# Performance work log

Hardware: AMD Instinct MI355X
Metric: run time of the kernel (lower is better)

Reference implementation:

```python
import jax, jax.numpy as jnp
import numpy as np

# attn_reps = "8x0n+30x1n": per head channel C = 8 scalars + 30 Lorentz four-vectors (4 each) = 128
N_SCALARS, N_VECTORS = 8, 30
ETA = jnp.diag(jnp.array([1.0, -1.0, -1.0, -1.0], dtype=jnp.float32))  # Minkowski metric


def _quat_to_rot(q):
    # q: (M,4) unit quaternions -> (M,3,3) rotation matrices
    w, x, y, z = q[:, 0], q[:, 1], q[:, 2], q[:, 3]
    r0 = jnp.stack([1 - 2 * (y * y + z * z), 2 * (x * y - w * z), 2 * (x * z + w * y)], axis=-1)
    r1 = jnp.stack([2 * (x * y + w * z), 1 - 2 * (x * x + z * z), 2 * (y * z - w * x)], axis=-1)
    r2 = jnp.stack([2 * (x * z - w * y), 2 * (y * z + w * x), 1 - 2 * (x * x + y * y)], axis=-1)
    return jnp.stack([r0, r1, r2], axis=-2)


def _random_lorentz(key, M):
    # random proper Lorentz transforms: boost(beta) @ blockdiag(1, R)
    k1, k2 = jax.random.split(key)
    quat = jax.random.normal(k1, (M, 4), dtype=jnp.float32)
    quat = quat / jnp.linalg.norm(quat, axis=-1, keepdims=True)
    R = _quat_to_rot(quat)  # (M,3,3)
    beta = jax.random.uniform(k2, (M, 3), minval=-1.0, maxval=1.0, dtype=jnp.float32) * (0.6 / np.sqrt(3.0))
    b2 = jnp.sum(beta * beta, axis=-1)  # (M,), < 0.36
    gamma = 1.0 / jnp.sqrt(1.0 - b2)
    n = beta / jnp.sqrt(jnp.maximum(b2, 1e-12))[:, None]
    gb = gamma[:, None] * beta  # (M,3)
    top = jnp.concatenate([gamma[:, None], gb], axis=-1)[:, None, :]  # (M,1,4)
    spatial = jnp.eye(3, dtype=jnp.float32) + (gamma - 1.0)[:, None, None] * n[:, :, None] * n[:, None, :]
    bottom = jnp.concatenate([gb[:, :, None], spatial], axis=-1)  # (M,3,4)
    B = jnp.concatenate([top, bottom], axis=-2)  # (M,4,4) boost
    rot4 = jnp.zeros((M, 4, 4), dtype=jnp.float32).at[:, 0, 0].set(1.0).at[:, 1:, 1:].set(R)
    return jnp.einsum('mij,mjk->mik', B, rot4)


def setup_inputs() -> dict:
    key = jax.random.key(0)
    kq, kk, kv, kl = jax.random.split(key, 4)
    B, H, N, C = 8, 8, 1024, 128
    q = jax.random.normal(kq, (B, H, N, C), dtype=jnp.float32)
    k = jax.random.normal(kk, (B, H, N, C), dtype=jnp.float32)
    v = jax.random.normal(kv, (B, H, N, C), dtype=jnp.float32)
    L = _random_lorentz(kl, B * N).reshape(B, N, 4, 4)
    return {"q_local": q, "k_local": k, "v_local": v, "lframes_matrices": L}


def _transform(x, M):
    # TensorRepsTransform: scalars pass through, four-vectors get v' = M v (per particle)
    # x: (B,H,N,C), M: (B,N,4,4)
    s = x[..., :N_SCALARS]
    vec = x[..., N_SCALARS:].reshape(x.shape[:-1] + (N_VECTORS, 4))
    vec = jnp.einsum('bnij,bhnvj->bhnvi', M, vec)
    return jnp.concatenate([s, vec.reshape(x.shape[:-1] + (N_VECTORS * 4,))], axis=-1)


def reference(q_local, k_local, v_local, lframes_matrices):
    C = q_local.shape[-1]
    # InverseLFrames: Lorentz inverse  Lambda^{-1} = eta Lambda^T eta
    inv = jnp.einsum('ij,bnkj,kl->bnil', ETA, lframes_matrices, ETA)
    # LowerIndices: lower the output index -> eta @ Lambda^{-1}
    lower_inv = jnp.einsum('ij,bnjk->bnik', ETA, inv)
    q_g = _transform(q_local, inv)
    k_g = _transform(k_local, lower_inv)
    v_g = _transform(v_local, inv)
    # standard SDPA (scale 1/sqrt(C))
    scores = jnp.einsum('bhqc,bhkc->bhqk', q_g, k_g) * (1.0 / np.sqrt(C))
    attn = jax.nn.softmax(scores, axis=-1)
    out_g = jnp.einsum('bhqk,bhkc->bhqc', attn, v_g)
    # back to local frame with Lambda itself
    return _transform(out_g, lframes_matrices)
```

## Files before the change

kernel.cpp:

```cpp
#include <hip/hip_runtime.h>
#include <math.h>

typedef _Float16 f16;
typedef _Float16 f16x4 __attribute__((ext_vector_type(4)));
typedef _Float16 f16x8 __attribute__((ext_vector_type(8)));
typedef float    f32x4 __attribute__((ext_vector_type(4)));

typedef const __attribute__((address_space(1))) void gv_t;
typedef __attribute__((address_space(3))) void lv_t;

#define NSEQ 1024
#define CD   128
#define LT   136


__global__ __launch_bounds__(256)
void ipa_pre(const float* __restrict__ kg, const float* __restrict__ vg,
             const float* __restrict__ Lm, f16* __restrict__ khs, f16* __restrict__ vhs)
{
    __shared__ float LL[64 * 16];
    __shared__ __align__(16) f16 Kt[64 * LT];
    __shared__ __align__(16) f16 Vt[64 * LT];
    const int bx = blockIdx.x, nt = blockIdx.y, tid = threadIdx.x;
    const int bh = ((bx & 7) << 3) | (bx >> 3);
    const int b  = bh >> 3;
    const float* Lb = Lm + ((size_t)b * NSEQ + nt * 64) * 16;
    for (int t = tid; t < 64 * 16; t += 256) LL[t] = Lb[t];
    __syncthreads();

    const size_t base = ((size_t)bh * NSEQ + nt * 64) * CD;
    #pragma unroll
    for (int it = 0; it < 8; ++it) {
        int g = it * 256 + tid;
        int row = g >> 5, cg = g & 31;
        size_t idx = base + row * CD + cg * 4;
        const float* Lr = &LL[row * 16];
        float4 xk = *(const float4*)(kg + idx);
        float4 xv = *(const float4*)(vg + idx);
        float4 yk = xk, yv = xv;
        if (cg >= 2) {
            float t0 = xk.x, t1 = -xk.y, t2 = -xk.z, t3 = -xk.w;
            yk.x = Lr[0]*t0 + Lr[4]*t1 + Lr[8] *t2 + Lr[12]*t3;
            yk.y = Lr[1]*t0 + Lr[5]*t1 + Lr[9] *t2 + Lr[13]*t3;
            yk.z = Lr[2]*t0 + Lr[6]*t1 + Lr[10]*t2 + Lr[14]*t3;
            yk.w = Lr[3]*t0 + Lr[7]*t1 + Lr[11]*t2 + Lr[15]*t3;
            t0 = xv.x; t1 = -xv.y; t2 = -xv.z; t3 = -xv.w;
            yv.x =  (Lr[0]*t0 + Lr[4]*t1 + Lr[8] *t2 + Lr[12]*t3);
            yv.y = -(Lr[1]*t0 + Lr[5]*t1 + Lr[9] *t2 + Lr[13]*t3);
            yv.z = -(Lr[2]*t0 + Lr[6]*t1 + Lr[10]*t2 + Lr[14]*t3);
            yv.w = -(Lr[3]*t0 + Lr[7]*t1 + Lr[11]*t2 + Lr[15]*t3);
        }
        f16x4 hk = {(f16)yk.x, (f16)yk.y, (f16)yk.z, (f16)yk.w};
        f16x4 hv = {(f16)yv.x, (f16)yv.y, (f16)yv.z, (f16)yv.w};
        *(f16x4*)&Kt[row * LT + cg * 4] = hk;
        *(f16x4*)&Vt[row * LT + cg * 4] = hv;
    }
    __syncthreads();

    f16* kout = khs + (size_t)bh * 131072 + (size_t)nt * 4 * 4 * 512;
    #pragma unroll
    for (int it = 0; it < 4; ++it) {
        int slot = it * 256 + tid;
        int g16l = slot >> 8, cs = (slot >> 6) & 3, L = slot & 63;
        int lq = L & 15, quad = L >> 4;
        int keyl = ((g16l >> 1) << 5) + ((lq >> 2) << 3) + ((g16l & 1) << 2) + (lq & 3);
        f16x8 kv = *(const f16x8*)&Kt[keyl * LT + cs * 32 + quad * 8];
        *(f16x8*)(kout + (g16l * 4 + cs) * 512 + L * 8) = kv;
    }
    f16* vout = vhs + (size_t)bh * 131072 + (size_t)nt * 2 * 8 * 512;
    #pragma unroll
    for (int it = 0; it < 4; ++it) {
        int slot = it * 256 + tid;
        int k32l = slot >> 9, cb = (slot >> 6) & 7, L = slot & 63;
        int lq = L & 15, quad = L >> 4;
        int c = cb * 16 + lq;
        f16x8 o;
        #pragma unroll
        for (int j = 0; j < 8; ++j)
            o[j] = Vt[(k32l * 32 + quad * 8 + j) * LT + c];
        *(f16x8*)(vout + (k32l * 8 + cb) * 512 + L * 8) = o;
    }
}

__global__ __launch_bounds__(256, 2)
void ipa_attn(const float* __restrict__ qg, const f16* __restrict__ khs,
              const f16* __restrict__ vhs, const float* __restrict__ Lm,
              float* __restrict__ out)
{
    __shared__ __align__(16) f16 sK[2][8192];
    __shared__ __align__(16) f16 sV[2][8192];
    const int n = blockIdx.x;
    const int bh = ((n & 7) << 3) | ((n >> 3) & 7);
    const int b  = bh >> 3;
    const int tid = threadIdx.x;
    const int w = tid >> 6, lane = tid & 63, lq = lane & 15, quad = lane >> 4;
    const int qblk = n >> 6;
    const int q0 = qblk * 128 + w * 32;
    const f16* kbh = khs + (size_t)bh * 131072;
    const f16* vbh = vhs + (size_t)bh * 131072;
    const float sc2 = 0.12751744154226873f;

    auto stage = [&](int nb, int it) {
        const char* kp = (const char*)(kbh + (size_t)it * 8192);
        const char* vp = (const char*)(vbh + (size_t)it * 8192);
        char* kd = (char*)&sK[nb][0];
        char* vd = (char*)&sV[nb][0];
        #pragma unroll
        for (int j = 0; j < 4; ++j) {
            int off = (w * 4 + j) * 1024;
            __builtin_amdgcn_global_load_lds((gv_t*)(kp + off + lane * 16),
                                             (lv_t*)(kd + off), 16, 0, 0);
            __builtin_amdgcn_global_load_lds((gv_t*)(vp + off + lane * 16),
                                             (lv_t*)(vd + off), 16, 0, 0);
        }
    };

    f16x8 qf[2][4];
    #pragma unroll
    for (int u = 0; u < 2; ++u) {
        int qrow = q0 + u * 16 + lq;
        const float* Lr = Lm + ((size_t)b * NSEQ + qrow) * 16;
        const float* qp = qg + ((size_t)bh * NSEQ + qrow) * CD;
        float Lv[16];
        #pragma unroll
        for (int i = 0; i < 4; ++i) *(float4*)&Lv[i*4] = *(const float4*)(Lr + i*4);
        #pragma unroll
        for (int cs = 0; cs < 4; ++cs) {
            int c0 = cs * 32 + quad * 8;
            float4 x0 = *(const float4*)(qp + c0);
            float4 x1 = *(const float4*)(qp + c0 + 4);
            if (c0 >= 8) {
                float t0 = x0.x, t1 = -x0.y, t2 = -x0.z, t3 = -x0.w;
                float4 y;
                y.x =  (Lv[0]*t0 + Lv[4]*t1 + Lv[8] *t2 + Lv[12]*t3);
                y.y = -(Lv[1]*t0 + Lv[5]*t1 + Lv[9] *t2 + Lv[13]*t3);
                y.z = -(Lv[2]*t0 + Lv[6]*t1 + Lv[10]*t2 + Lv[14]*t3);
                y.w = -(Lv[3]*t0 + Lv[7]*t1 + Lv[11]*t2 + Lv[15]*t3);
                x0 = y;
                t0 = x1.x; t1 = -x1.y; t2 = -x1.z; t3 = -x1.w;
                y.x =  (Lv[0]*t0 + Lv[4]*t1 + Lv[8] *t2 + Lv[12]*t3);
                y.y = -(Lv[1]*t0 + Lv[5]*t1 + Lv[9] *t2 + Lv[13]*t3);
                y.z = -(Lv[2]*t0 + Lv[6]*t1 + Lv[10]*t2 + Lv[14]*t3);
                y.w = -(Lv[3]*t0 + Lv[7]*t1 + Lv[11]*t2 + Lv[15]*t3);
                x1 = y;
            }
            qf[u][cs] = (f16x8){(f16)(x0.x*sc2), (f16)(x0.y*sc2), (f16)(x0.z*sc2), (f16)(x0.w*sc2),
                                (f16)(x1.x*sc2), (f16)(x1.y*sc2), (f16)(x1.z*sc2), (f16)(x1.w*sc2)};
        }
    }

    f32x4 oacc[2][8];
    #pragma unroll
    for (int u = 0; u < 2; ++u)
        #pragma unroll
        for (int cb = 0; cb < 8; ++cb) oacc[u][cb] = (f32x4){0.f, 0.f, 0.f, 0.f};
    float mrun[2] = {-1e30f, -1e30f}, lrun[2] = {0.f, 0.f};

    stage(0, 0);

    for (int it = 0; it < 16; ++it) {
        const int cur = it & 1;
        __syncthreads();
        if (it < 15) stage(cur ^ 1, it + 1);

        const f16* kb = &sK[cur][0];
        const f16* vb = &sV[cur][0];
        f16x8 kf[4][4];
        #pragma unroll
        for (int g = 0; g < 4; ++g)
            #pragma unroll
            for (int cs = 0; cs < 4; ++cs)
                kf[g][cs] = *(const f16x8*)&kb[(g * 4 + cs) * 512 + lane * 8];

        f32x4 s[2][4];
        #pragma unroll
        for (int u = 0; u < 2; ++u)
            #pragma unroll
            for (int g = 0; g < 4; ++g) s[u][g] = (f32x4){0.f, 0.f, 0.f, 0.f};
        #pragma unroll
        for (int g = 0; g < 4; ++g)
            #pragma unroll
            for (int cs = 0; cs < 4; ++cs) {
                s[0][g] = __builtin_amdgcn_mfma_f32_16x16x32_f16(kf[g][cs], qf[0][cs], s[0][g], 0, 0, 0);
                s[1][g] = __builtin_amdgcn_mfma_f32_16x16x32_f16(kf[g][cs], qf[1][cs], s[1][g], 0, 0, 0);
            }

        f16x8 vf[2][8];
        #pragma unroll
        for (int k2 = 0; k2 < 2; ++k2)
            #pragma unroll
            for (int cb = 0; cb < 8; ++cb)
                vf[k2][cb] = *(const f16x8*)&vb[(k2 * 8 + cb) * 512 + lane * 8];

        f16x8 pf[2][2];
        #pragma unroll
        for (int u = 0; u < 2; ++u) {
            float mx = -1e30f;
            #pragma unroll
            for (int g = 0; g < 4; ++g)
                mx = fmaxf(mx, fmaxf(fmaxf(s[u][g].x, s[u][g].y), fmaxf(s[u][g].z, s[u][g].w)));
            mx = fmaxf(mx, __shfl_xor(mx, 16, 64));
            mx = fmaxf(mx, __shfl_xor(mx, 32, 64));
            float mnew = fmaxf(mrun[u], mx);
            if (!__all(mx <= mrun[u])) {
                float alpha = exp2f(mrun[u] - mnew);
                lrun[u] *= alpha;
                #pragma unroll
                for (int cb = 0; cb < 8; ++cb) oacc[u][cb] *= alpha;
                mrun[u] = mnew;
            }
            float p[16], rs = 0.f;
            #pragma unroll
            for (int g = 0; g < 4; ++g) {
                p[g*4+0] = exp2f(s[u][g].x - mnew);
                p[g*4+1] = exp2f(s[u][g].y - mnew);
                p[g*4+2] = exp2f(s[u][g].z - mnew);
                p[g*4+3] = exp2f(s[u][g].w - mnew);
                rs += (p[g*4+0] + p[g*4+1]) + (p[g*4+2] + p[g*4+3]);
            }
            rs += __shfl_xor(rs, 16, 64);
            rs += __shfl_xor(rs, 32, 64);
            lrun[u] += rs;
            pf[u][0] = (f16x8){(f16)p[0],(f16)p[1],(f16)p[2],(f16)p[3],(f16)p[4],(f16)p[5],(f16)p[6],(f16)p[7]};
            pf[u][1] = (f16x8){(f16)p[8],(f16)p[9],(f16)p[10],(f16)p[11],(f16)p[12],(f16)p[13],(f16)p[14],(f16)p[15]};
        }
        #pragma unroll
        for (int k2 = 0; k2 < 2; ++k2)
            #pragma unroll
            for (int cb = 0; cb < 8; ++cb) {
                oacc[0][cb] = __builtin_amdgcn_mfma_f32_16x16x32_f16(vf[k2][cb], pf[0][k2], oacc[0][cb], 0, 0, 0);
                oacc[1][cb] = __builtin_amdgcn_mfma_f32_16x16x32_f16(vf[k2][cb], pf[1][k2], oacc[1][cb], 0, 0, 0);
            }
    }

    #pragma unroll
    for (int u = 0; u < 2; ++u) {
        int qrow = q0 + u * 16 + lq;
        float invl = 1.0f / lrun[u];
        const float* Lr = Lm + ((size_t)b * NSEQ + qrow) * 16;
        float* ob = out + ((size_t)bh * NSEQ + qrow) * CD;
        #pragma unroll
        for (int cb = 0; cb < 8; ++cb) {
            int c0 = cb * 16 + quad * 4;
            float o0 = oacc[u][cb].x*invl, o1 = oacc[u][cb].y*invl;
            float o2 = oacc[u][cb].z*invl, o3 = oacc[u][cb].w*invl;
            float4 r;
            if (c0 >= 8) {
                r.x = Lr[0] *o0 + Lr[1] *o1 + Lr[2] *o2 + Lr[3] *o3;
                r.y = Lr[4] *o0 + Lr[5] *o1 + Lr[6] *o2 + Lr[7] *o3;
                r.z = Lr[8] *o0 + Lr[9] *o1 + Lr[10]*o2 + Lr[11]*o3;
                r.w = Lr[12]*o0 + Lr[13]*o1 + Lr[14]*o2 + Lr[15]*o3;
            } else {
                r.x = o0; r.y = o1; r.z = o2; r.w = o3;
            }
            *(float4*)(ob + c0) = r;
        }
    }
}

extern "C" void kernel_launch(void* const* d_in, const int* in_sizes, int n_in,
                              void* d_out, int out_size, void* d_ws, size_t ws_size,
                              hipStream_t stream) {
    const float* q = (const float*)d_in[0];
    const float* k = (const float*)d_in[1];
    const float* v = (const float*)d_in[2];
    const float* L = (const float*)d_in[3];
    float* o = (float*)d_out;
    f16* khs = (f16*)d_ws;
    f16* vhs = khs + (size_t)64 * 131072;
    dim3 grid1(64, 16);
    ipa_pre<<<grid1, 256, 0, stream>>>(k, v, L, khs, vhs);
    ipa_attn<<<512, 256, 0, stream>>>(q, khs, vhs, L, o);
}
```

Baseline: 190.3 us.

## Halve attention query and KV tile sizes and double the grid

```diff
diff --git a/kernel.cpp b/kernel.cpp
--- a/kernel.cpp
+++ b/kernel.cpp
@@ -87,27 +87,27 @@
               const f16* __restrict__ vhs, const float* __restrict__ Lm,
               float* __restrict__ out)
 {
-    __shared__ __align__(16) f16 sK[2][8192];
-    __shared__ __align__(16) f16 sV[2][8192];
+    __shared__ __align__(16) f16 sK[2][4096];
+    __shared__ __align__(16) f16 sV[2][4096];
     const int n = blockIdx.x;
     const int bh = ((n & 7) << 3) | ((n >> 3) & 7);
     const int b  = bh >> 3;
     const int tid = threadIdx.x;
     const int w = tid >> 6, lane = tid & 63, lq = lane & 15, quad = lane >> 4;
     const int qblk = n >> 6;
-    const int q0 = qblk * 128 + w * 32;
+    const int q0 = qblk * 64 + w * 16;
     const f16* kbh = khs + (size_t)bh * 131072;
     const f16* vbh = vhs + (size_t)bh * 131072;
     const float sc2 = 0.12751744154226873f;
 
     auto stage = [&](int nb, int it) {
-        const char* kp = (const char*)(kbh + (size_t)it * 8192);
-        const char* vp = (const char*)(vbh + (size_t)it * 8192);
+        const char* kp = (const char*)(kbh + (size_t)it * 4096);
+        const char* vp = (const char*)(vbh + (size_t)it * 4096);
         char* kd = (char*)&sK[nb][0];
         char* vd = (char*)&sV[nb][0];
         #pragma unroll
-        for (int j = 0; j < 4; ++j) {
-            int off = (w * 4 + j) * 1024;
+        for (int j = 0; j < 2; ++j) {
+            int off = (w * 2 + j) * 1024;
             __builtin_amdgcn_global_load_lds((gv_t*)(kp + off + lane * 16),
                                              (lv_t*)(kd + off), 16, 0, 0);
             __builtin_amdgcn_global_load_lds((gv_t*)(vp + off + lane * 16),
@@ -115,10 +115,9 @@
         }
     };
 
-    f16x8 qf[2][4];
-    #pragma unroll
-    for (int u = 0; u < 2; ++u) {
-        int qrow = q0 + u * 16 + lq;
+    f16x8 qf[4];
+    {
+        int qrow = q0 + lq;
         const float* Lr = Lm + ((size_t)b * NSEQ + qrow) * 16;
         const float* qp = qg + ((size_t)bh * NSEQ + qrow) * CD;
         float Lv[16];
@@ -144,106 +143,78 @@
                 y.w = -(Lv[3]*t0 + Lv[7]*t1 + Lv[11]*t2 + Lv[15]*t3);
                 x1 = y;
             }
-            qf[u][cs] = (f16x8){(f16)(x0.x*sc2), (f16)(x0.y*sc2), (f16)(x0.z*sc2), (f16)(x0.w*sc2),
-                                (f16)(x1.x*sc2), (f16)(x1.y*sc2), (f16)(x1.z*sc2), (f16)(x1.w*sc2)};
-        }
-    }
-
-    f32x4 oacc[2][8];
-    #pragma unroll
-    for (int u = 0; u < 2; ++u)
-        #pragma unroll
-        for (int cb = 0; cb < 8; ++cb) oacc[u][cb] = (f32x4){0.f, 0.f, 0.f, 0.f};
-    float mrun[2] = {-1e30f, -1e30f}, lrun[2] = {0.f, 0.f};
+            qf[cs] = (f16x8){(f16)(x0.x*sc2), (f16)(x0.y*sc2), (f16)(x0.z*sc2), (f16)(x0.w*sc2),
+                             (f16)(x1.x*sc2), (f16)(x1.y*sc2), (f16)(x1.z*sc2), (f16)(x1.w*sc2)};
+        }
+    }
+
+    f32x4 oacc[8];
+    #pragma unroll
+    for (int cb = 0; cb < 8; ++cb) oacc[cb] = (f32x4){0.f, 0.f, 0.f, 0.f};
+    float mrun = -1e30f, lrun = 0.f;
 
     stage(0, 0);
 
-    for (int it = 0; it < 16; ++it) {
+    for (int it = 0; it < 32; ++it) {
         const int cur = it & 1;
         __syncthreads();
-        if (it < 15) stage(cur ^ 1, it + 1);
+        if (it < 31) stage(cur ^ 1, it + 1);
 
         const f16* kb = &sK[cur][0];
         const f16* vb = &sV[cur][0];
-        f16x8 kf[4][4];
-        #pragma unroll
-        for (int g = 0; g < 4; ++g)
+
+        f32x4 s[2];
+        s[0] = (f32x4){0.f, 0.f, 0.f, 0.f};
+        s[1] = (f32x4){0.f, 0.f, 0.f, 0.f};
+        #pragma unroll
+        for (int cs = 0; cs < 4; ++cs) {
+            f16x8 kf0 = *(const f16x8*)&kb[(cs    ) * 512 + lane * 8];
+            f16x8 kf1 = *(const f16x8*)&kb[(cs + 4) * 512 + lane * 8];
+            s[0] = __builtin_amdgcn_mfma_f32_16x16x32_f16(kf0, qf[cs], s[0], 0, 0, 0);
+            s[1] = __builtin_amdgcn_mfma_f32_16x16x32_f16(kf1, qf[cs], s[1], 0, 0, 0);
+        }
+
+        float mx = fmaxf(fmaxf(fmaxf(s[0].x, s[0].y), fmaxf(s[0].z, s[0].w)),
+                         fmaxf(fmaxf(s[1].x, s[1].y), fmaxf(s[1].z, s[1].w)));
+        mx = fmaxf(mx, __shfl_xor(mx, 16, 64));
+        mx = fmaxf(mx, __shfl_xor(mx, 32, 64));
+        float mnew = fmaxf(mrun, mx);
+        if (!__all(mx <= mrun)) {
+            float alpha = exp2f(mrun - mnew);
+            lrun *= alpha;
             #pragma unroll
-            for (int cs = 0; cs < 4; ++cs)
-                kf[g][cs] = *(const f16x8*)&kb[(g * 4 + cs) * 512 + lane * 8];
-
-        f32x4 s[2][4];
-        #pragma unroll
-        for (int u = 0; u < 2; ++u)
-            #pragma unroll
-            for (int g = 0; g < 4; ++g) s[u][g] = (f32x4){0.f, 0.f, 0.f, 0.f};
-        #pragma unroll
-        for (int g = 0; g < 4; ++g)
-            #pragma unroll
-            for (int cs = 0; cs < 4; ++cs) {
-                s[0][g] = __builtin_amdgcn_mfma_f32_16x16x32_f16(kf[g][cs], qf[0][cs], s[0][g], 0, 0, 0);
-                s[1][g] = __builtin_amdgcn_mfma_f32_16x16x32_f16(kf[g][cs], qf[1][cs], s[1][g], 0, 0, 0);
-            }
-
-        f16x8 vf[2][8];
-        #pragma unroll
-        for (int k2 = 0; k2 < 2; ++k2)
-            #pragma unroll
-            for (int cb = 0; cb < 8; ++cb)
-                vf[k2][cb] = *(const f16x8*)&vb[(k2 * 8 + cb) * 512 + lane * 8];
-
-        f16x8 pf[2][2];
-        #pragma unroll
-        for (int u = 0; u < 2; ++u) {
-            float mx = -1e30f;
-            #pragma unroll
-            for (int g = 0; g < 4; ++g)
-                mx = fmaxf(mx, fmaxf(fmaxf(s[u][g].x, s[u][g].y), fmaxf(s[u][g].z, s[u][g].w)));
-            mx = fmaxf(mx, __shfl_xor(mx, 16, 64));
-            mx = fmaxf(mx, __shfl_xor(mx, 32, 64));
-            float mnew = fmaxf(mrun[u], mx);
-            if (!__all(mx <= mrun[u])) {
-                float alpha = exp2f(mrun[u] - mnew);
-                lrun[u] *= alpha;
-                #pragma unroll
-                for (int cb = 0; cb < 8; ++cb) oacc[u][cb] *= alpha;
-                mrun[u] = mnew;
-            }
-            float p[16], rs = 0.f;
-            #pragma unroll
-            for (int g = 0; g < 4; ++g) {
-                p[g*4+0] = exp2f(s[u][g].x - mnew);
-                p[g*4+1] = exp2f(s[u][g].y - mnew);
-                p[g*4+2] = exp2f(s[u][g].z - mnew);
-                p[g*4+3] = exp2f(s[u][g].w - mnew);
-                rs += (p[g*4+0] + p[g*4+1]) + (p[g*4+2] + p[g*4+3]);
-            }
-            rs += __shfl_xor(rs, 16, 64);
-            rs += __shfl_xor(rs, 32, 64);
-            lrun[u] += rs;
-            pf[u][0] = (f16x8){(f16)p[0],(f16)p[1],(f16)p[2],(f16)p[3],(f16)p[4],(f16)p[5],(f16)p[6],(f16)p[7]};
-            pf[u][1] = (f16x8){(f16)p[8],(f16)p[9],(f16)p[10],(f16)p[11],(f16)p[12],(f16)p[13],(f16)p[14],(f16)p[15]};
-        }
-        #pragma unroll
-        for (int k2 = 0; k2 < 2; ++k2)
-            #pragma unroll
-            for (int cb = 0; cb < 8; ++cb) {
-                oacc[0][cb] = __builtin_amdgcn_mfma_f32_16x16x32_f16(vf[k2][cb], pf[0][k2], oacc[0][cb], 0, 0, 0);
-                oacc[1][cb] = __builtin_amdgcn_mfma_f32_16x16x32_f16(vf[k2][cb], pf[1][k2], oacc[1][cb], 0, 0, 0);
-            }
-    }
-
-    #pragma unroll
-    for (int u = 0; u < 2; ++u) {
-        int qrow = q0 + u * 16 + lq;
-        float invl = 1.0f / lrun[u];
+            for (int cb = 0; cb < 8; ++cb) oacc[cb] *= alpha;
+            mrun = mnew;
+        }
+        float p[8];
+        p[0] = exp2f(s[0].x - mnew); p[1] = exp2f(s[0].y - mnew);
+        p[2] = exp2f(s[0].z - mnew); p[3] = exp2f(s[0].w - mnew);
+        p[4] = exp2f(s[1].x - mnew); p[5] = exp2f(s[1].y - mnew);
+        p[6] = exp2f(s[1].z - mnew); p[7] = exp2f(s[1].w - mnew);
+        lrun += ((p[0]+p[1]) + (p[2]+p[3])) + ((p[4]+p[5]) + (p[6]+p[7]));
+        f16x8 pf = {(f16)p[0],(f16)p[1],(f16)p[2],(f16)p[3],
+                    (f16)p[4],(f16)p[5],(f16)p[6],(f16)p[7]};
+
+        #pragma unroll
+        for (int cb = 0; cb < 8; ++cb) {
+            f16x8 vf = *(const f16x8*)&vb[cb * 512 + lane * 8];
+            oacc[cb] = __builtin_amdgcn_mfma_f32_16x16x32_f16(vf, pf, oacc[cb], 0, 0, 0);
+        }
+    }
+
+    {
+        float l = lrun;
+        l += __shfl_xor(l, 16, 64);
+        l += __shfl_xor(l, 32, 64);
+        float invl = 1.0f / l;
+        int qrow = q0 + lq;
         const float* Lr = Lm + ((size_t)b * NSEQ + qrow) * 16;
         float* ob = out + ((size_t)bh * NSEQ + qrow) * CD;
         #pragma unroll
         for (int cb = 0; cb < 8; ++cb) {
             int c0 = cb * 16 + quad * 4;
-            float o0 = oacc[u][cb].x*invl, o1 = oacc[u][cb].y*invl;
-            float o2 = oacc[u][cb].z*invl, o3 = oacc[u][cb].w*invl;
+            float o0 = oacc[cb].x*invl, o1 = oacc[cb].y*invl;
+            float o2 = oacc[cb].z*invl, o3 = oacc[cb].w*invl;
             float4 r;
             if (c0 >= 8) {
                 r.x = Lr[0] *o0 + Lr[1] *o1 + Lr[2] *o2 + Lr[3] *o3;
@@ -270,5 +241,5 @@
     f16* vhs = khs + (size_t)64 * 131072;
     dim3 grid1(64, 16);
     ipa_pre<<<grid1, 256, 0, stream>>>(k, v, L, khs, vhs);
-    ipa_attn<<<512, 256, 0, stream>>>(q, khs, vhs, L, o);
+    ipa_attn<<<1024, 256, 0, stream>>>(q, khs, vhs, L, o);
 }
```

Result: slower. 196.5 us (+3.3%).
